# Kernel tuning notes

Measured on AMD Instinct MI355X. Metric: run time of the kernel, lower is better.

Reference implementation:

```python
import jax, jax.numpy as jnp
import numpy as np

D_MODEL = 1024
N_HEADS = 16
D_HEAD = D_MODEL // N_HEADS          # 64
ROT_DIM = D_HEAD // 2                # 32, rotary dim (lucidrains dim arg)
THETA = 10000.0
BATCH, SEQ = 4, 4096


def _rope(t):
    """lucidrains rotate_queries_or_keys with seq_dim=-2, applied to t of shape (H,B,dh,S).
    Positions run along the dh axis (size D_HEAD); rotation touches only the first
    ROT_DIM entries of the last axis (S); the rest passes through unchanged."""
    inv_freq = 1.0 / (THETA ** (jnp.arange(0, ROT_DIM, 2, dtype=jnp.float32) / ROT_DIM))  # (ROT_DIM//2,)
    pos = jnp.arange(D_HEAD, dtype=jnp.float32)                                           # (dh,)
    freqs = pos[:, None] * inv_freq[None, :]                                              # (dh, ROT_DIM//2)
    freqs = jnp.repeat(freqs, 2, axis=-1)                                                 # (dh, ROT_DIM) interleaved f0,f0,f1,f1
    cos, sin = jnp.cos(freqs), jnp.sin(freqs)                                             # broadcast over (H,B,dh,ROT_DIM)
    t_rot, t_pass = t[..., :ROT_DIM], t[..., ROT_DIM:]
    x1, x2 = t_rot[..., 0::2], t_rot[..., 1::2]
    rot_half = jnp.stack((-x2, x1), axis=-1).reshape(t_rot.shape)                         # rotate_half (adjacent pairs)
    t_rot = t_rot * cos + rot_half * sin
    return jnp.concatenate([t_rot, t_pass], axis=-1)


def setup_inputs() -> dict:
    key = jax.random.key(0)
    k1, k2, k3 = jax.random.split(key, 3)
    x = jax.random.normal(k1, (BATCH, SEQ, D_MODEL), jnp.float32)
    W = jax.random.normal(k2, (3 * D_MODEL, D_MODEL), jnp.float32) * (D_MODEL ** -0.5)  # torch Linear weight layout
    b = jax.random.normal(k3, (3 * D_MODEL,), jnp.float32) * 0.01
    return {"x": x, "W": W, "b": b}


def reference(x, W, b):
    B, S, _ = x.shape
    qkv = x @ W.T + b                                            # (B,S,3D)
    qkv = qkv.reshape(B, S, N_HEADS, 3 * D_HEAD).transpose(2, 0, 3, 1)  # (H,B,3dh,S)
    q, k, v = jnp.split(qkv, 3, axis=-2)                         # each (H,B,dh,S)
    q = _rope(q)
    k = _rope(k)
    scale = D_HEAD ** -0.5
    scores = jnp.einsum('hbds,hbes->hbde', q, k) * scale         # (H,B,dh,dh) — contracts over S
    probs = jax.nn.softmax(scores, axis=-1)
    out = jnp.einsum('hbde,hbes->hbds', probs, v)                # (H,B,dh,S)
    out = out.transpose(0, 2, 1, 3).reshape(B, S, N_HEADS * D_HEAD)  # faithful to torch transpose(1,2).reshape
    return out
```

## Files before the change

### kernel.cpp

```cpp
#include <hip/hip_runtime.h>
#include <stdint.h>

#define D_MODEL 1024
#define N_HEADS 16
#define D_HEAD  64
#define BATCH   4
#define SEQ     4096
#define BS      (BATCH*SEQ)
#define QKV_N   (3*D_MODEL)
#define HB      (N_HEADS*BATCH)
#define NCHUNK  8
#define CH_S    (SEQ/NCHUNK)

using f16x8 = __attribute__((ext_vector_type(8))) _Float16;
using f32x4 = __attribute__((ext_vector_type(4))) float;
using i32x4 = __attribute__((ext_vector_type(4))) int;
typedef __attribute__((address_space(3))) ushort AS3U;

__device__ static inline ushort f2h(float f) {
    _Float16 h = (_Float16)f; ushort u; __builtin_memcpy(&u, &h, 2); return u;
}
__device__ static inline void async16(const ushort* g, ushort* l) {
    __builtin_amdgcn_global_load_lds(
        (const __attribute__((address_space(1))) void*)g,
        (__attribute__((address_space(3))) void*)l, 16, 0, 0);
}

__global__ __launch_bounds__(256)
void cvt_both(const float* __restrict__ x, const float* __restrict__ W,
              ushort* __restrict__ xh, ushort* __restrict__ Wh, int nx)
{
    int i = (blockIdx.x * 256 + threadIdx.x) * 8;
    const float* src; ushort* dst; int o;
    if (i < nx) { src = x; dst = xh; o = i; }
    else        { src = W; dst = Wh; o = i - nx; }
    float4 a = *(const float4*)(src + o);
    float4 b = *(const float4*)(src + o + 4);
    *(ushort4*)(dst + o)     = make_ushort4(f2h(a.x),f2h(a.y),f2h(a.z),f2h(a.w));
    *(ushort4*)(dst + o + 4) = make_ushort4(f2h(b.x),f2h(b.y),f2h(b.z),f2h(b.w));
}

#define MF(a,b,c) __builtin_amdgcn_mfma_f32_16x16x32_f16(a,b,c,0,0,0)
#define FENCE asm volatile("" ::: "memory")
#define VM0 asm volatile("s_waitcnt vmcnt(0)" ::: "memory")

#define DSR(D, P, IMM) do { i32x4 _t; \
    asm volatile("ds_read_b128 %0, %1 offset:%2" : "=v"(_t) : "v"(P), "n"(IMM)); \
    D = __builtin_bit_cast(f16x8, _t); } while (0)

#define STAGE_AB(NXT, KT) do { \
    async16(aS0 + (KT)*32, &lds[(NXT)*4096 + d0]); \
    async16(aS1 + (KT)*32, &lds[(NXT)*4096 + d1]); \
    async16(bS0 + (KT)*32, &lds[8192 + (NXT)*4096 + d0]); \
    async16(bS1 + (KT)*32, &lds[8192 + (NXT)*4096 + d1]); } while (0)

#define STEP(CUR, STG) do { \
    STG; \
    const AS3U* pa = lA + (CUR)*4096; \
    const AS3U* pb = lB + (CUR)*4096; \
    f16x8 a0,a1,a2,a3,b0,b1,b2,b3; \
    DSR(a0, pa, 0); DSR(a1, pa, 1024); DSR(a2, pa, 2048); DSR(a3, pa, 3072); \
    DSR(b0, pb, 0); DSR(b1, pb, 1024); DSR(b2, pb, 2048); DSR(b3, pb, 3072); \
    asm volatile("s_waitcnt lgkmcnt(0)" ::: "memory"); \
    __builtin_amdgcn_sched_barrier(0); \
    __builtin_amdgcn_s_setprio(1); \
    if (!isV) { \
        acc[0][0]=MF(a0,b0,acc[0][0]); acc[0][1]=MF(a0,b1,acc[0][1]); \
        acc[0][2]=MF(a0,b2,acc[0][2]); acc[0][3]=MF(a0,b3,acc[0][3]); \
        acc[1][0]=MF(a1,b0,acc[1][0]); acc[1][1]=MF(a1,b1,acc[1][1]); \
        acc[1][2]=MF(a1,b2,acc[1][2]); acc[1][3]=MF(a1,b3,acc[1][3]); \
        acc[2][0]=MF(a2,b0,acc[2][0]); acc[2][1]=MF(a2,b1,acc[2][1]); \
        acc[2][2]=MF(a2,b2,acc[2][2]); acc[2][3]=MF(a2,b3,acc[2][3]); \
        acc[3][0]=MF(a3,b0,acc[3][0]); acc[3][1]=MF(a3,b1,acc[3][1]); \
        acc[3][2]=MF(a3,b2,acc[3][2]); acc[3][3]=MF(a3,b3,acc[3][3]); \
    } else { \
        acc[0][0]=MF(b0,a0,acc[0][0]); acc[0][1]=MF(b1,a0,acc[0][1]); \
        acc[0][2]=MF(b2,a0,acc[0][2]); acc[0][3]=MF(b3,a0,acc[0][3]); \
        acc[1][0]=MF(b0,a1,acc[1][0]); acc[1][1]=MF(b1,a1,acc[1][1]); \
        acc[1][2]=MF(b2,a1,acc[1][2]); acc[1][3]=MF(b3,a1,acc[1][3]); \
        acc[2][0]=MF(b0,a2,acc[2][0]); acc[2][1]=MF(b1,a2,acc[2][1]); \
        acc[2][2]=MF(b2,a2,acc[2][2]); acc[2][3]=MF(b3,a2,acc[2][3]); \
        acc[3][0]=MF(b0,a3,acc[3][0]); acc[3][1]=MF(b1,a3,acc[3][1]); \
        acc[3][2]=MF(b2,a3,acc[3][2]); acc[3][3]=MF(b3,a3,acc[3][3]); \
    } \
    __builtin_amdgcn_s_setprio(0); \
    VM0; \
    FENCE; __builtin_amdgcn_s_barrier(); FENCE; \
  } while (0)

__global__ __launch_bounds__(256)
void qkv_gemm_f16(const ushort* __restrict__ Ah, const ushort* __restrict__ Bh,
                  const float* __restrict__ bias,
                  ushort* __restrict__ qh, ushort* __restrict__ kh,
                  ushort* __restrict__ varr)
{
    __shared__ ushort lds[4 * 4096];
    const int t = threadIdx.x;
    const int lane = t & 63, w = t >> 6;

    const int id0 = blockIdx.y * 24 + blockIdx.x;
    const int ids = (id0 & 7) * 384 + (id0 >> 3);
    const int n0 = (ids % 24) * 128;
    const int m0 = (ids / 24) * 128;

    const int wm = (w >> 1) * 64;
    const int wn = (w & 1) * 64;
    const int fr = lane & 15;
    const int hq = lane >> 4;

    const int u0 = t, u1 = 256 + t;
    const int rp0 = u0 >> 3, rp1 = u1 >> 3;
    const int sl0 = (u0 & 7) ^ (rp0 & 7), sl1 = (u1 & 7) ^ (rp1 & 7);
    const int r0 = rp0 * 2 + (sl0 >> 2), r1 = rp1 * 2 + (sl1 >> 2);
    const int c0 = (sl0 & 3) * 8,        c1 = (sl1 & 3) * 8;
    const ushort* aS0 = Ah + (size_t)(m0 + r0) * D_MODEL + c0;
    const ushort* aS1 = Ah + (size_t)(m0 + r1) * D_MODEL + c1;
    const ushort* bS0 = Bh + (size_t)(n0 + r0) * D_MODEL + c0;
    const ushort* bS1 = Bh + (size_t)(n0 + r1) * D_MODEL + c1;
    const int d0 = w * 512;
    const int d1 = 2048 + w * 512;

    const int rdo  = ((fr >> 1) * 64) + ((((fr & 1) * 4 + hq) ^ ((fr >> 1) & 7)) * 8);
    const AS3U* lA = (const AS3U*)lds + (wm * 32 + rdo);
    const AS3U* lB = (const AS3U*)lds + (8192 + wn * 32 + rdo);

    const int cgb = n0 + wn;
    const int typ = __builtin_amdgcn_readfirstlane((cgb % 192) / 64);
    const bool isV = (typ == 2);

    f32x4 acc[4][4] = {};

    STAGE_AB(0, 0);
    VM0;
    __builtin_amdgcn_s_barrier();
    FENCE;

    #pragma unroll 1
    for (int it = 0; it < 15; ++it) {
        STEP(0, STAGE_AB(1, 2*it + 1));
        STEP(1, STAGE_AB(0, 2*it + 2));
    }
    STEP(0, STAGE_AB(1, 31));
    STEP(1, );

    const int col = lane & 15, rq = (lane >> 4) * 4;
    const int h   = cgb / 192;
    const int b   = m0 >> 12;
    const int sbl = (m0 & 4095) + wm;

    if (typ < 2) {
        ushort* dst = typ ? kh : qh;
        #pragma unroll
        for (int j = 0; j < 4; ++j) {
            const int ci = j*16 + col;
            const float bj = bias[cgb + ci];
            const size_t rowoff = ((size_t)(h*4 + b)*64 + ci) * SEQ;
            #pragma unroll
            for (int i = 0; i < 4; ++i) {
                const int s0 = sbl + i*16 + rq;
                float v0 = acc[i][j][0] + bj, v1 = acc[i][j][1] + bj;
                float v2 = acc[i][j][2] + bj, v3 = acc[i][j][3] + bj;
                if (s0 < 32) {
                    int mp = s0 >> 1;
                    float if0 = __expf(-0.5756462732485115f * (float)mp);
                    float if1 = __expf(-0.5756462732485115f * (float)(mp + 1));
                    float a0 = (float)ci * if0, a1 = (float)ci * if1;
                    float cc0 = __cosf(a0), s0n = __sinf(a0);
                    float cc1 = __cosf(a1), s1n = __sinf(a1);
                    float n0_ = v0*cc0 - v1*s0n, n1_ = v1*cc0 + v0*s0n;
                    float n2_ = v2*cc1 - v3*s1n, n3_ = v3*cc1 + v2*s1n;
                    v0 = n0_; v1 = n1_; v2 = n2_; v3 = n3_;
                }
                *(ushort4*)&dst[rowoff + s0] = make_ushort4(
                    f2h(v0), f2h(v1), f2h(v2), f2h(v3));
            }
        }
    } else {
        const size_t base = (size_t)(h*4 + b) * SEQ;
        #pragma unroll
        for (int j = 0; j < 4; ++j) {
            const float4 b4 = *(const float4*)&bias[cgb + j*16 + rq];
            #pragma unroll
            for (int i = 0; i < 4; ++i) {
                const int s = sbl + i*16 + col;
                *(ushort4*)&varr[(base + s)*64 + j*16 + rq] = make_ushort4(
                    f2h(acc[i][j][0] + b4.x), f2h(acc[i][j][1] + b4.y),
                    f2h(acc[i][j][2] + b4.z), f2h(acc[i][j][3] + b4.w));
            }
        }
    }
}

__global__ __launch_bounds__(256)
void scores_partial(const ushort* __restrict__ qh, const ushort* __restrict__ kh,
                    float* __restrict__ partial)
{
    __shared__ float L[4 * 4096];
    const int t = threadIdx.x, lane = t & 63, w = t >> 6;
    const int hb = blockIdx.x, chunk = blockIdx.y;
    const ushort* qb = qh + (size_t)hb * 64 * SEQ;
    const ushort* kb = kh + (size_t)hb * 64 * SEQ;
    const int fr = lane & 15, fq = (lane >> 4) * 8;

    f32x4 acc[4][4] = {};
    const int kbase = chunk * CH_S + w * (CH_S / 4);
    for (int kk = 0; kk < CH_S / 4; kk += 32) {
        const int k0 = kbase + kk;
        f16x8 af[4], bf[4];
        #pragma unroll
        for (int i = 0; i < 4; ++i)
            af[i] = *(const f16x8*)&qb[(size_t)(i*16 + fr) * SEQ + k0 + fq];
        #pragma unroll
        for (int j = 0; j < 4; ++j)
            bf[j] = *(const f16x8*)&kb[(size_t)(j*16 + fr) * SEQ + k0 + fq];
        #pragma unroll
        for (int i = 0; i < 4; ++i)
            #pragma unroll
            for (int j = 0; j < 4; ++j)
                acc[i][j] = __builtin_amdgcn_mfma_f32_16x16x32_f16(
                                af[i], bf[j], acc[i][j], 0, 0, 0);
    }

    float* Lw = &L[w * 4096];
    const int col = lane & 15, rq = (lane >> 4) * 4;
    #pragma unroll
    for (int i = 0; i < 4; ++i)
        #pragma unroll
        for (int j = 0; j < 4; ++j)
            #pragma unroll
            for (int r = 0; r < 4; ++r)
                Lw[(i*16 + rq + r)*64 + j*16 + col] = acc[i][j][r];
    __syncthreads();

    float* pb = partial + ((size_t)hb * NCHUNK + chunk) * 4096;
    #pragma unroll
    for (int u = 0; u < 4; ++u) {
        int idx = u*1024 + t*4;
        f32x4 s = *(f32x4*)&L[idx];
        s += *(f32x4*)&L[4096 + idx];
        s += *(f32x4*)&L[8192 + idx];
        s += *(f32x4*)&L[12288 + idx];
        *(f32x4*)&pb[idx] = s;
    }
}

__global__ __launch_bounds__(256)
void softmax_k(const float* __restrict__ partial, ushort* __restrict__ Pt)
{
    __shared__ float L[64 * 65];
    const int t = threadIdx.x;
    const int hb = blockIdx.x;
    const float* pb = partial + (size_t)hb * NCHUNK * 4096;

    #pragma unroll
    for (int u = 0; u < 16; ++u) {
        int idx = u*256 + t;
        float s = 0.f;
        #pragma unroll
        for (int c = 0; c < NCHUNK; ++c) s += pb[c*4096 + idx];
        L[(idx >> 6) * 65 + (idx & 63)] = s;
    }
    __syncthreads();

    if (t < 64) {
        float* row = &L[t * 65];
        float mx = -1e30f;
        for (int e = 0; e < 64; ++e) mx = fmaxf(mx, row[e]);
        float sum = 0.f;
        for (int e = 0; e < 64; ++e) {
            float v = expf(0.125f * (row[e] - mx));
            row[e] = v; sum += v;
        }
        float inv = 1.f / sum;
        ushort* pd = Pt + (size_t)hb * 4096 + t * 64;
        for (int e = 0; e < 64; ++e) pd[e] = f2h(row[e] * inv);
    }
}

__global__ __launch_bounds__(256)
void attn_out_mfma(const ushort* __restrict__ varr, const ushort* __restrict__ Pt,
                   float* __restrict__ out)
{
    const int t = threadIdx.x, lane = t & 63, w = t >> 6;
    const int hb = blockIdx.x;
    const int sb = blockIdx.y * 256 + w * 64;
    const int fr = lane & 15, fq = (lane >> 4) * 8;

    const ushort* Pb = Pt + (size_t)hb * 4096;
    const ushort* vb = varr + (size_t)hb * SEQ * 64;

    f16x8 aV[4][2], bP[4][2];
    #pragma unroll
    for (int i = 0; i < 4; ++i)
        #pragma unroll
        for (int ks = 0; ks < 2; ++ks)
            aV[i][ks] = *(const f16x8*)&vb[(size_t)(sb + i*16 + fr)*64 + ks*32 + fq];
    #pragma unroll
    for (int j = 0; j < 4; ++j)
        #pragma unroll
        for (int ks = 0; ks < 2; ++ks)
            bP[j][ks] = *(const f16x8*)&Pb[(j*16 + fr)*64 + ks*32 + fq];

    f32x4 acc[4][4] = {};
    #pragma unroll
    for (int ks = 0; ks < 2; ++ks)
        #pragma unroll
        for (int i = 0; i < 4; ++i)
            #pragma unroll
            for (int j = 0; j < 4; ++j)
                acc[i][j] = __builtin_amdgcn_mfma_f32_16x16x32_f16(
                                aV[i][ks], bP[j][ks], acc[i][j], 0, 0, 0);

    const int col = lane & 15, rq = (lane >> 4) * 4;
    const int h = hb >> 2, b = hb & 3;
    #pragma unroll
    for (int i = 0; i < 4; ++i)
        #pragma unroll
        for (int j = 0; j < 4; ++j) {
            const int dg = j*16 + col;
            size_t off = (((size_t)h*64 + dg)*4 + b)*SEQ + sb + i*16 + rq;
            *(float4*)&out[off] = make_float4(acc[i][j][0], acc[i][j][1],
                                              acc[i][j][2], acc[i][j][3]);
        }
}

extern "C" void kernel_launch(void* const* d_in, const int* in_sizes, int n_in,
                              void* d_out, int out_size, void* d_ws, size_t ws_size,
                              hipStream_t stream)
{
    const float* x    = (const float*)d_in[0];
    const float* W    = (const float*)d_in[1];
    const float* bias = (const float*)d_in[2];
    float* out = (float*)d_out;

    char* p = (char*)d_ws;
    ushort* qh   = (ushort*)p;  p += (size_t)HB * 64 * SEQ * 2;
    ushort* kh   = (ushort*)p;  p += (size_t)HB * 64 * SEQ * 2;
    ushort* varr = (ushort*)p;  p += (size_t)HB * SEQ * 64 * 2;
    ushort* Pth  = (ushort*)p;  p += (size_t)HB * 4096 * 2;
    float* partial = (float*)p; p += (size_t)HB * NCHUNK * 4096 * 4;
    ushort* xh   = (ushort*)p;  p += (size_t)BS * D_MODEL * 2;
    ushort* Wh   = (ushort*)p;  p += (size_t)QKV_N * D_MODEL * 2;

    const int nx = BS * D_MODEL;
    const int nw = QKV_N * D_MODEL;
    cvt_both<<<(nx + nw)/2048, 256, 0, stream>>>(x, W, xh, Wh, nx);

    qkv_gemm_f16<<<dim3(QKV_N/128, BS/128), 256, 0, stream>>>(
        xh, Wh, bias, qh, kh, varr);

    scores_partial<<<dim3(HB, NCHUNK), 256, 0, stream>>>(qh, kh, partial);
    softmax_k<<<HB, 256, 0, stream>>>(partial, Pth);
    attn_out_mfma<<<dim3(HB, 16), 256, 0, stream>>>(varr, Pth, out);
}
```

Before: 315.6 us.

## Fuse softmax into attention-output kernel and halve score split chunks

Result: faster. 298.2 us (-5.5%).

```diff
diff --git a/kernel.cpp b/kernel.cpp
--- a/kernel.cpp
+++ b/kernel.cpp
@@ -9,7 +9,7 @@
 #define BS      (BATCH*SEQ)
 #define QKV_N   (3*D_MODEL)
 #define HB      (N_HEADS*BATCH)
-#define NCHUNK  8
+#define NCHUNK  4
 #define CH_S    (SEQ/NCHUNK)
 
 using f16x8 = __attribute__((ext_vector_type(8))) _Float16;
@@ -245,48 +245,44 @@
 }
 
 __global__ __launch_bounds__(256)
-void softmax_k(const float* __restrict__ partial, ushort* __restrict__ Pt)
-{
-    __shared__ float L[64 * 65];
-    const int t = threadIdx.x;
-    const int hb = blockIdx.x;
-    const float* pb = partial + (size_t)hb * NCHUNK * 4096;
-
-    #pragma unroll
-    for (int u = 0; u < 16; ++u) {
-        int idx = u*256 + t;
-        float s = 0.f;
-        #pragma unroll
-        for (int c = 0; c < NCHUNK; ++c) s += pb[c*4096 + idx];
-        L[(idx >> 6) * 65 + (idx & 63)] = s;
-    }
-    __syncthreads();
-
-    if (t < 64) {
-        float* row = &L[t * 65];
-        float mx = -1e30f;
-        for (int e = 0; e < 64; ++e) mx = fmaxf(mx, row[e]);
-        float sum = 0.f;
-        for (int e = 0; e < 64; ++e) {
-            float v = expf(0.125f * (row[e] - mx));
-            row[e] = v; sum += v;
-        }
-        float inv = 1.f / sum;
-        ushort* pd = Pt + (size_t)hb * 4096 + t * 64;
-        for (int e = 0; e < 64; ++e) pd[e] = f2h(row[e] * inv);
-    }
-}
-
-__global__ __launch_bounds__(256)
-void attn_out_mfma(const ushort* __restrict__ varr, const ushort* __restrict__ Pt,
+void attn_out_mfma(const ushort* __restrict__ varr, const float* __restrict__ partial,
                    float* __restrict__ out)
 {
+    __shared__ ushort P_lds[64 * 72];
     const int t = threadIdx.x, lane = t & 63, w = t >> 6;
     const int hb = blockIdx.x;
     const int sb = blockIdx.y * 256 + w * 64;
     const int fr = lane & 15, fq = (lane >> 4) * 8;
 
-    const ushort* Pb = Pt + (size_t)hb * 4096;
+    {
+        const float* pb = partial + (size_t)hb * NCHUNK * 4096;
+        const int row = t >> 2, l4 = t & 3;
+        const int eb = row*64 + l4*16;
+        float s[16];
+        #pragma unroll
+        for (int i = 0; i < 16; ++i) {
+            float a = 0.f;
+            #pragma unroll
+            for (int c = 0; c < NCHUNK; ++c) a += pb[c*4096 + eb + i];
+            s[i] = a * 0.125f;
+        }
+        float mx = s[0];
+        #pragma unroll
+        for (int i = 1; i < 16; ++i) mx = fmaxf(mx, s[i]);
+        mx = fmaxf(mx, __shfl_xor(mx, 1));
+        mx = fmaxf(mx, __shfl_xor(mx, 2));
+        float sum = 0.f;
+        #pragma unroll
+        for (int i = 0; i < 16; ++i) { s[i] = __expf(s[i] - mx); sum += s[i]; }
+        sum += __shfl_xor(sum, 1);
+        sum += __shfl_xor(sum, 2);
+        const float inv = 1.f / sum;
+        #pragma unroll
+        for (int i = 0; i < 16; ++i)
+            P_lds[row*72 + l4*16 + i] = f2h(s[i] * inv);
+    }
+    __syncthreads();
+
     const ushort* vb = varr + (size_t)hb * SEQ * 64;
 
     f16x8 aV[4][2], bP[4][2];
@@ -299,7 +295,7 @@
     for (int j = 0; j < 4; ++j)
         #pragma unroll
         for (int ks = 0; ks < 2; ++ks)
-            bP[j][ks] = *(const f16x8*)&Pb[(j*16 + fr)*64 + ks*32 + fq];
+            bP[j][ks] = *(const f16x8*)&P_lds[(j*16 + fr)*72 + ks*32 + fq];
 
     f32x4 acc[4][4] = {};
     #pragma unroll
@@ -337,7 +333,6 @@
     ushort* qh   = (ushort*)p;  p += (size_t)HB * 64 * SEQ * 2;
     ushort* kh   = (ushort*)p;  p += (size_t)HB * 64 * SEQ * 2;
     ushort* varr = (ushort*)p;  p += (size_t)HB * SEQ * 64 * 2;
-    ushort* Pth  = (ushort*)p;  p += (size_t)HB * 4096 * 2;
     float* partial = (float*)p; p += (size_t)HB * NCHUNK * 4096 * 4;
     ushort* xh   = (ushort*)p;  p += (size_t)BS * D_MODEL * 2;
     ushort* Wh   = (ushort*)p;  p += (size_t)QKV_N * D_MODEL * 2;
@@ -350,6 +345,5 @@
         xh, Wh, bias, qh, kh, varr);
 
     scores_partial<<<dim3(HB, NCHUNK), 256, 0, stream>>>(qh, kh, partial);
-    softmax_k<<<HB, 256, 0, stream>>>(partial, Pth);
-    attn_out_mfma<<<dim3(HB, 16), 256, 0, stream>>>(varr, Pth, out);
-}
+    attn_out_mfma<<<dim3(HB, 16), 256, 0, stream>>>(varr, partial, out);
+}
```
